# Performance work log

Hardware: AMD Instinct MI355X
Metric: run time of the kernel (lower is better)

Reference implementation:

```python
import jax, jax.numpy as jnp
import numpy as np


def ctc_neg_log_likelihood(log_probs, labels, input_lengths, label_lengths, blank=0):
    """Per-sample CTC negative log likelihood (torch.nn.CTCLoss semantics,
    zero_infinity=True). log_probs: (T, B, V) log-softmax; labels: (B, L) int."""
    T, B, V = log_probs.shape
    L = labels.shape[1]
    S = 2 * L + 1  # extended label sequence with interleaved blanks
    NEG = jnp.asarray(-1e9, log_probs.dtype)
    # extended labels: blank at even positions, label at odd positions -> (B, S)
    ext = jnp.full((B, S), blank, dtype=labels.dtype).at[:, 1::2].set(labels)
    # log prob of each extended symbol at each time: (T, B, S)
    lp_ext = jnp.take_along_axis(log_probs, jnp.broadcast_to(ext[None].astype(jnp.int32), (T, B, S)), axis=2)
    # skip transition s-2 -> s allowed iff ext[s] != blank and ext[s] != ext[s-2]
    skip = jnp.concatenate(
        [jnp.zeros((B, 2), bool), (ext[:, 2:] != blank) & (ext[:, 2:] != ext[:, :-2])], axis=1)
    alpha0 = jnp.full((B, S), NEG).at[:, 0].set(lp_ext[0, :, 0]).at[:, 1].set(lp_ext[0, :, 1])

    def step(alpha, inp):
        lp_t, t = inp
        s1 = jnp.concatenate([jnp.full((B, 1), NEG), alpha[:, :-1]], axis=1)
        s2 = jnp.where(skip, jnp.concatenate([jnp.full((B, 2), NEG), alpha[:, :-2]], axis=1), NEG)
        new = jnp.logaddexp(jnp.logaddexp(alpha, s1), s2) + lp_t
        # frames beyond each sample's input length leave alpha unchanged
        alpha = jnp.where((t < input_lengths)[:, None], new, alpha)
        return alpha, None

    alpha, _ = jax.lax.scan(step, alpha0, (lp_ext[1:], jnp.arange(1, T)))
    i1 = (2 * label_lengths.astype(jnp.int32) - 1)[:, None]
    a_last = jnp.take_along_axis(alpha, i1, axis=1)[:, 0]
    a_blank = jnp.take_along_axis(alpha, i1 + 1, axis=1)[:, 0]
    nll = -jnp.logaddexp(a_last, a_blank)
    # zero_infinity=True: infeasible alignments contribute 0
    return jnp.where(nll > 1e8, jnp.zeros_like(nll), nll)


def setup_inputs() -> dict:
    B, T, D, V, L = 32, 2048, 512, 5, 256
    key = jax.random.key(0)
    k1, k2, k3, k4, k5 = jax.random.split(key, 5)
    hs_pad = jax.random.normal(k1, (B, T, D), dtype=jnp.float32)
    W = jax.random.normal(k2, (D, V), dtype=jnp.float32) * 0.02
    b = jnp.zeros((V,), dtype=jnp.float32)
    hlens = jax.random.randint(k3, (B,), 1024, T + 1, dtype=jnp.int32)
    ys_pad = jax.random.randint(k4, (B, L), 1, V, dtype=jnp.int32)  # labels never equal blank=0
    ys_lens = jax.random.randint(k5, (B,), 64, L + 1, dtype=jnp.int32)
    return {"hs_pad": hs_pad, "W": W, "b": b, "hlens": hlens, "ys_pad": ys_pad, "ys_lens": ys_lens}


def reference(hs_pad, W, b, hlens, ys_pad, ys_lens):
    B = hs_pad.shape[0]
    logits = jnp.einsum('btd,dv->btv', hs_pad, W) + b      # ctc_lo (dropout p=0)
    logits_tbv = jnp.transpose(logits, (1, 0, 2))          # (T, B, V)
    log_probs = jax.nn.log_softmax(logits_tbv, axis=2)
    probs = jnp.exp(log_probs)                             # == softmax(logits)
    per_sample = ctc_neg_log_likelihood(log_probs, ys_pad, hlens, ys_lens, blank=0)
    loss = jnp.sum(per_sample) / B                         # sum-reduced CTC / batch size
    ys_hat = jnp.transpose(log_probs, (1, 0, 2))           # (B, T, V)
    no_log_ys_hat = jnp.transpose(probs, (1, 0, 2))        # (B, T, V)
    return loss, ys_hat, no_log_ys_hat
```

## Files before the change

### kernel.cpp

```cpp
#include <hip/hip_runtime.h>
#include <math.h>

#define B_DIM 32
#define T_DIM 2048
#define D_DIM 512
#define V_DIM 5
#define L_DIM 256
#define LN2D 0.6931471805599453
#define TP (T_DIM + 4)

typedef const float __attribute__((address_space(1)))* gas_fp;
typedef float __attribute__((address_space(3)))* las_fp;

__device__ __forceinline__ double dpp_shr1_f64(double x) {
    int lo = __double2loint(x), hi = __double2hiint(x);
    int slo = __builtin_amdgcn_update_dpp(0, lo, 0x138, 0xf, 0xf, true);
    int shi = __builtin_amdgcn_update_dpp(0, hi, 0x138, 0xf, 0xf, true);
    return __hiloint2double(shi, slo);
}
__device__ __forceinline__ int wave_imax_dpp(int e) {
    e = max(e, __builtin_amdgcn_update_dpp(0, e, 0x111, 0xf, 0xf, true));
    e = max(e, __builtin_amdgcn_update_dpp(0, e, 0x112, 0xf, 0xf, true));
    e = max(e, __builtin_amdgcn_update_dpp(0, e, 0x114, 0xf, 0xf, true));
    e = max(e, __builtin_amdgcn_update_dpp(0, e, 0x118, 0xf, 0xf, true));
    e = max(e, __builtin_amdgcn_update_dpp(0, e, 0x142, 0xf, 0xf, true));
    e = max(e, __builtin_amdgcn_update_dpp(0, e, 0x143, 0xf, 0xf, true));
    return __builtin_amdgcn_readlane(e, 63);
}
__device__ __forceinline__ float wave_fsum_dpp(float x) {
    x += __int_as_float(__builtin_amdgcn_update_dpp(0, __float_as_int(x), 0x111, 0xf, 0xf, true));
    x += __int_as_float(__builtin_amdgcn_update_dpp(0, __float_as_int(x), 0x112, 0xf, 0xf, true));
    x += __int_as_float(__builtin_amdgcn_update_dpp(0, __float_as_int(x), 0x114, 0xf, 0xf, true));
    x += __int_as_float(__builtin_amdgcn_update_dpp(0, __float_as_int(x), 0x118, 0xf, 0xf, true));
    x += __int_as_float(__builtin_amdgcn_update_dpp(0, __float_as_int(x), 0x142, 0xa, 0xf, false));
    x += __int_as_float(__builtin_amdgcn_update_dpp(0, __float_as_int(x), 0x143, 0xc, 0xf, false));
    return x;
}

__global__ __launch_bounds__(256) void k_logits_softmax(
    const float* __restrict__ hs, const float* __restrict__ W,
    const float* __restrict__ bias, float* __restrict__ logp,
    float* __restrict__ probs)
{
    const int lane = threadIdx.x & 63;
    const int wid  = (blockIdx.x * blockDim.x + threadIdx.x) >> 6;
    const int nwav = (gridDim.x * blockDim.x) >> 6;

    float wr[2][4][V_DIM];
#pragma unroll
    for (int c = 0; c < 2; ++c)
#pragma unroll
        for (int j = 0; j < 4; ++j) {
            const int k = c * 256 + lane * 4 + j;
#pragma unroll
            for (int v = 0; v < V_DIM; ++v) wr[c][j][v] = W[k * V_DIM + v];
        }
    float br[V_DIM];
#pragma unroll
    for (int v = 0; v < V_DIM; ++v) br[v] = bias[v];

    for (int row = wid; row < B_DIM * T_DIM; row += nwav) {
        const float* x = hs + (size_t)row * D_DIM;
        float4 xa = *reinterpret_cast<const float4*>(x + lane * 4);
        float4 xb = *reinterpret_cast<const float4*>(x + 256 + lane * 4);
        const float xs0[4] = {xa.x, xa.y, xa.z, xa.w};
        const float xs1[4] = {xb.x, xb.y, xb.z, xb.w};

        float acc[V_DIM];
#pragma unroll
        for (int v = 0; v < V_DIM; ++v) acc[v] = 0.f;
#pragma unroll
        for (int j = 0; j < 4; ++j)
#pragma unroll
            for (int v = 0; v < V_DIM; ++v) {
                acc[v] = fmaf(xs0[j], wr[0][j][v], acc[v]);
                acc[v] = fmaf(xs1[j], wr[1][j][v], acc[v]);
            }
#pragma unroll
        for (int v = 0; v < V_DIM; ++v) acc[v] = wave_fsum_dpp(acc[v]);

        if (lane == 63) {
#pragma unroll
            for (int v = 0; v < V_DIM; ++v) acc[v] += br[v];
            float m = fmaxf(fmaxf(fmaxf(acc[0], acc[1]), fmaxf(acc[2], acc[3])), acc[4]);
            float e[V_DIM], s = 0.f;
#pragma unroll
            for (int v = 0; v < V_DIM; ++v) { e[v] = __expf(acc[v] - m); s += e[v]; }
            float lse = m + __logf(s);
            float inv = 1.f / s;
            size_t base = (size_t)row * V_DIM;
#pragma unroll
            for (int v = 0; v < V_DIM; ++v) {
                logp[base + v]  = acc[v] - lse;
                probs[base + v] = e[v] * inv;
            }
        }
    }
}

__global__ __launch_bounds__(64) void k_ctc(
    const float* __restrict__ probs, const int* __restrict__ ys_pad,
    const int* __restrict__ hlens, const int* __restrict__ ys_lens,
    float* __restrict__ nll_out)
{
    __shared__ float  s_probs[T_DIM * V_DIM];
    __shared__ __align__(16) double s_pT[4][TP];
    __shared__ double s_alpha[513];
    __shared__ double s_red[64];

    const int b    = blockIdx.x;
    const int lane = threadIdx.x;
    const int hlen = hlens[b];
    const int lb   = ys_lens[b];
    const int Sb   = 2 * lb + 1;
    const float* pb = probs + (size_t)b * T_DIM * V_DIM;
    const int*  yrow = ys_pad + b * L_DIM;

    for (int i = 0; i < (T_DIM * V_DIM) / 64; ++i) {
        __builtin_amdgcn_global_load_lds((gas_fp)(pb + i * 64 + lane),
                                         (las_fp)(&s_probs[i * 64]), 4, 0, 0);
    }
    asm volatile("s_waitcnt vmcnt(0)" ::: "memory");

    double lg2 = 0.0;
    for (int i = 0; i < T_DIM / 64; ++i) {
        const int t = i * 64 + lane;
        const float* sp = &s_probs[t * 5];
        const float p0 = sp[0];
        const float inv = 1.0f / p0;
        s_pT[0][t + 3] = (double)(sp[1] * inv);
        s_pT[1][t + 3] = (double)(sp[2] * inv);
        s_pT[2][t + 3] = (double)(sp[3] * inv);
        s_pT[3][t + 3] = (double)(sp[4] * inv);
        if (t < hlen) {
            int ee; float mm = frexpf(p0, &ee);
            lg2 += (double)ee + (double)__log2f(mm);
        }
    }

    const int y0 = yrow[4 * lane + 0];
    const int y1 = yrow[4 * lane + 1];
    const int y2 = yrow[4 * lane + 2];
    const int y3 = yrow[4 * lane + 3];
    const int ym1 = (lane > 0) ? yrow[4 * lane - 1] : -1;

    const double sk0 = ((lane > 0) && (y0 != ym1)) ? 1.0 : 0.0;
    const double sk1 = (y1 != y0) ? 1.0 : 0.0;
    const double sk2 = (y2 != y1) ? 1.0 : 0.0;
    const double sk3 = (y3 != y2) ? 1.0 : 0.0;

    bool vmask[9];
#pragma unroll
    for (int i = 0; i < 9; ++i) vmask[i] = (8 * lane + i) < Sb;

    double aA[9], aB[9];
#pragma unroll
    for (int i = 0; i < 9; ++i) aA[i] = 0.0;
    if (lane == 0) {
        aA[0] = 1.0;
        aA[1] = s_pT[y0 - 1][3];
    }
    int E = 0;

    const double* q_y0 = &s_pT[y0 - 1][0];
    const double* q_y1 = &s_pT[y1 - 1][0];
    const double* q_y2 = &s_pT[y2 - 1][0];
    const double* q_y3 = &s_pT[y3 - 1][0];

#define LD4(d, p)                                                         \
    { double2 u0_ = *(const double2*)(p);                                 \
      double2 u1_ = *(const double2*)((p) + 2);                           \
      (d)[0] = u0_.x; (d)[1] = u0_.y; (d)[2] = u1_.x; (d)[3] = u1_.y; }

#define LOADQ(dst, kk)                                                    \
    { const int off_ = 4 + 4 * (kk);                                      \
      LD4(dst + 0,  q_y0 + off_); LD4(dst + 4,  q_y1 + off_);             \
      LD4(dst + 8,  q_y2 + off_); LD4(dst + 12, q_y3 + off_); }

#define STEPX(O, N, L, s_)                                                \
    {                                                                     \
        double p7_ = dpp_shr1_f64(O[7]);                                  \
        N[7] = fma(sk3, O[5], O[7] + O[6]) * L[12 + (s_)];                \
        N[2] = O[2] + O[1];                                               \
        N[3] = fma(sk1, O[1], O[3] + O[2]) * L[4 + (s_)];                 \
        N[4] = O[4] + O[3];                                               \
        N[5] = fma(sk2, O[3], O[5] + O[4]) * L[8 + (s_)];                 \
        N[6] = O[6] + O[5];                                               \
        N[8] = O[8] + O[7];                                               \
        N[0] = O[0] + p7_;                                                \
        N[1] = fma(sk0, p7_, O[1] + O[0]) * L[0 + (s_)];                  \
    }

#define STEP4(L)                                                          \
    STEPX(aA, aB, L, 0); STEPX(aB, aA, L, 1);                             \
    STEPX(aA, aB, L, 2); STEPX(aB, aA, L, 3);

#define RENORM()                                                          \
    {                                                                     \
        int hm_ = 0;                                                      \
        _Pragma("unroll")                                                 \
        for (int i_ = 0; i_ < 9; ++i_) {                                  \
            int h_ = __double2hiint(aA[i_]);                              \
            hm_ = vmask[i_] ? max(hm_, h_) : hm_;                         \
        }                                                                 \
        int em_ = wave_imax_dpp(hm_) >> 20;                               \
        if (em_ > 0) {                                                    \
            double sc_ = __hiloint2double((2046 - em_) << 20, 0);         \
            _Pragma("unroll")                                             \
            for (int i_ = 0; i_ < 9; ++i_) aA[i_] *= sc_;                 \
            E += em_ - 1023;                                              \
        }                                                                 \
    }

    const int NS = hlen - 1;
    const int nfull = NS >> 2;
    double lpA[16], lpB[16];
    LOADQ(lpA, 0);

    int blk = 0;
    for (; blk + 2 <= nfull; blk += 2) {
        LOADQ(lpB, blk + 1);
        STEP4(lpA);
        LOADQ(lpA, blk + 2);
        STEP4(lpB);
        if (blk & 2) RENORM();
    }
    if (blk < nfull) {
        STEP4(lpA);
    }
    for (int tt = 4 * nfull + 1; tt <= NS; ++tt) {
        double lt[16];
        lt[0]  = s_pT[y0 - 1][tt + 3];
        lt[4]  = s_pT[y1 - 1][tt + 3];
        lt[8]  = s_pT[y2 - 1][tt + 3];
        lt[12] = s_pT[y3 - 1][tt + 3];
        STEPX(aA, aB, lt, 0);
#pragma unroll
        for (int i = 0; i < 9; ++i) aA[i] = aB[i];
    }

#pragma unroll
    for (int i = 0; i < 8; ++i) s_alpha[8 * lane + i] = aA[i];
    if (lane == 63) s_alpha[512] = aA[8];
    s_red[lane] = lg2;
    __syncthreads();
    if (lane == 0) {
        double lg2tot = 0.0;
        for (int i = 0; i < 64; ++i) lg2tot += s_red[i];
        int i1 = 2 * lb - 1;
        double s = s_alpha[i1] + s_alpha[i1 + 1];
        double nlld = -(log(s) + ((double)E + lg2tot) * LN2D);
        float nll = (float)nlld;
        if (!(nll < 1e8f)) nll = 0.f;
        nll_out[b] = nll;
    }
#undef STEPX
#undef STEP4
#undef LOADQ
#undef LD4
#undef RENORM
}

__global__ __launch_bounds__(64) void k_finalize(
    const float* __restrict__ nll, float* __restrict__ out)
{
    int tid = threadIdx.x;
    float v = (tid < B_DIM) ? nll[tid] : 0.f;
#pragma unroll
    for (int off = 32; off; off >>= 1) v += __shfl_down(v, off, 64);
    if (tid == 0) out[0] = v / (float)B_DIM;
}

extern "C" void kernel_launch(void* const* d_in, const int* in_sizes, int n_in,
                              void* d_out, int out_size, void* d_ws, size_t ws_size,
                              hipStream_t stream) {
    const float* hs      = (const float*)d_in[0];
    const float* W       = (const float*)d_in[1];
    const float* bias    = (const float*)d_in[2];
    const int*   hlens   = (const int*)d_in[3];
    const int*   ys_pad  = (const int*)d_in[4];
    const int*   ys_lens = (const int*)d_in[5];

    float* out   = (float*)d_out;
    float* logp  = out + 1;
    float* probs = out + 1 + (size_t)B_DIM * T_DIM * V_DIM;
    float* nll   = (float*)d_ws;

    hipLaunchKernelGGL(k_logits_softmax, dim3(1024), dim3(256), 0, stream,
                       hs, W, bias, logp, probs);
    hipLaunchKernelGGL(k_ctc, dim3(B_DIM), dim3(64), 0, stream,
                       probs, ys_pad, hlens, ys_lens, nll);
    hipLaunchKernelGGL(k_finalize, dim3(1), dim3(64), 0, stream, nll, out);
}
```

Measured before the change: 143.6 us.

## Switch CTC forward recursion to fp32 with per-lane exponent scaling

Moves the CTC alpha recursion from double to float. Each lane now keeps its own power-of-two exponent, and the value shifted in from the neighbouring lane is corrected with ldexpf using the exponent difference between lanes. Renormalisation now runs every 8 steps as a lane-local operation instead of a wave-wide max reduction, and the final log-likelihood combines the two end states using their per-lane exponents. This targets the cost of fp64 arithmetic on the serial critical path and halves shared-memory traffic, but adds an ldexp per step and risks underflow or precision loss in float.

```diff
diff --git a/kernel.cpp b/kernel.cpp
--- a/kernel.cpp
+++ b/kernel.cpp
@@ -12,20 +12,12 @@
 typedef const float __attribute__((address_space(1)))* gas_fp;
 typedef float __attribute__((address_space(3)))* las_fp;
 
-__device__ __forceinline__ double dpp_shr1_f64(double x) {
-    int lo = __double2loint(x), hi = __double2hiint(x);
-    int slo = __builtin_amdgcn_update_dpp(0, lo, 0x138, 0xf, 0xf, true);
-    int shi = __builtin_amdgcn_update_dpp(0, hi, 0x138, 0xf, 0xf, true);
-    return __hiloint2double(shi, slo);
-}
-__device__ __forceinline__ int wave_imax_dpp(int e) {
-    e = max(e, __builtin_amdgcn_update_dpp(0, e, 0x111, 0xf, 0xf, true));
-    e = max(e, __builtin_amdgcn_update_dpp(0, e, 0x112, 0xf, 0xf, true));
-    e = max(e, __builtin_amdgcn_update_dpp(0, e, 0x114, 0xf, 0xf, true));
-    e = max(e, __builtin_amdgcn_update_dpp(0, e, 0x118, 0xf, 0xf, true));
-    e = max(e, __builtin_amdgcn_update_dpp(0, e, 0x142, 0xf, 0xf, true));
-    e = max(e, __builtin_amdgcn_update_dpp(0, e, 0x143, 0xf, 0xf, true));
-    return __builtin_amdgcn_readlane(e, 63);
+__device__ __forceinline__ float dpp_shr1_f32(float x) {
+    return __int_as_float(__builtin_amdgcn_update_dpp(
+        0, __float_as_int(x), 0x138, 0xf, 0xf, true));
+}
+__device__ __forceinline__ int dpp_shr1_i32(int x) {
+    return __builtin_amdgcn_update_dpp(0, x, 0x138, 0xf, 0xf, true);
 }
 __device__ __forceinline__ float wave_fsum_dpp(float x) {
     x += __int_as_float(__builtin_amdgcn_update_dpp(0, __float_as_int(x), 0x111, 0xf, 0xf, true));
@@ -104,8 +96,9 @@
     float* __restrict__ nll_out)
 {
     __shared__ float  s_probs[T_DIM * V_DIM];
-    __shared__ __align__(16) double s_pT[4][TP];
-    __shared__ double s_alpha[513];
+    __shared__ __align__(16) float s_pT[4][TP];
+    __shared__ float  s_beta[513];
+    __shared__ int    s_E[64];
     __shared__ double s_red[64];
 
     const int b    = blockIdx.x;
@@ -128,10 +121,10 @@
         const float* sp = &s_probs[t * 5];
         const float p0 = sp[0];
         const float inv = 1.0f / p0;
-        s_pT[0][t + 3] = (double)(sp[1] * inv);
-        s_pT[1][t + 3] = (double)(sp[2] * inv);
-        s_pT[2][t + 3] = (double)(sp[3] * inv);
-        s_pT[3][t + 3] = (double)(sp[4] * inv);
+        s_pT[0][t + 3] = sp[1] * inv;
+        s_pT[1][t + 3] = sp[2] * inv;
+        s_pT[2][t + 3] = sp[3] * inv;
+        s_pT[3][t + 3] = sp[4] * inv;
         if (t < hlen) {
             int ee; float mm = frexpf(p0, &ee);
             lg2 += (double)ee + (double)__log2f(mm);
@@ -144,51 +137,51 @@
     const int y3 = yrow[4 * lane + 3];
     const int ym1 = (lane > 0) ? yrow[4 * lane - 1] : -1;
 
-    const double sk0 = ((lane > 0) && (y0 != ym1)) ? 1.0 : 0.0;
-    const double sk1 = (y1 != y0) ? 1.0 : 0.0;
-    const double sk2 = (y2 != y1) ? 1.0 : 0.0;
-    const double sk3 = (y3 != y2) ? 1.0 : 0.0;
+    const float sk0 = ((lane > 0) && (y0 != ym1)) ? 1.f : 0.f;
+    const float sk1 = (y1 != y0) ? 1.f : 0.f;
+    const float sk2 = (y2 != y1) ? 1.f : 0.f;
+    const float sk3 = (y3 != y2) ? 1.f : 0.f;
 
     bool vmask[9];
 #pragma unroll
     for (int i = 0; i < 9; ++i) vmask[i] = (8 * lane + i) < Sb;
 
-    double aA[9], aB[9];
-#pragma unroll
-    for (int i = 0; i < 9; ++i) aA[i] = 0.0;
+    float aA[9], aB[9];
+#pragma unroll
+    for (int i = 0; i < 9; ++i) aA[i] = 0.f;
     if (lane == 0) {
-        aA[0] = 1.0;
+        aA[0] = 1.f;
         aA[1] = s_pT[y0 - 1][3];
     }
     int E = 0;
-
-    const double* q_y0 = &s_pT[y0 - 1][0];
-    const double* q_y1 = &s_pT[y1 - 1][0];
-    const double* q_y2 = &s_pT[y2 - 1][0];
-    const double* q_y3 = &s_pT[y3 - 1][0];
-
-#define LD4(d, p)                                                         \
-    { double2 u0_ = *(const double2*)(p);                                 \
-      double2 u1_ = *(const double2*)((p) + 2);                           \
-      (d)[0] = u0_.x; (d)[1] = u0_.y; (d)[2] = u1_.x; (d)[3] = u1_.y; }
+    int delta = 0;
+
+    const float* q_y0 = &s_pT[y0 - 1][0];
+    const float* q_y1 = &s_pT[y1 - 1][0];
+    const float* q_y2 = &s_pT[y2 - 1][0];
+    const float* q_y3 = &s_pT[y3 - 1][0];
+
+#define LD4F(d, p)                                                        \
+    { float4 u_ = *(const float4*)(p);                                    \
+      (d)[0] = u_.x; (d)[1] = u_.y; (d)[2] = u_.z; (d)[3] = u_.w; }
 
 #define LOADQ(dst, kk)                                                    \
     { const int off_ = 4 + 4 * (kk);                                      \
-      LD4(dst + 0,  q_y0 + off_); LD4(dst + 4,  q_y1 + off_);             \
-      LD4(dst + 8,  q_y2 + off_); LD4(dst + 12, q_y3 + off_); }
+      LD4F(dst + 0,  q_y0 + off_); LD4F(dst + 4,  q_y1 + off_);           \
+      LD4F(dst + 8,  q_y2 + off_); LD4F(dst + 12, q_y3 + off_); }
 
 #define STEPX(O, N, L, s_)                                                \
     {                                                                     \
-        double p7_ = dpp_shr1_f64(O[7]);                                  \
-        N[7] = fma(sk3, O[5], O[7] + O[6]) * L[12 + (s_)];                \
+        float p7_ = ldexpf(dpp_shr1_f32(O[7]), delta);                    \
+        N[7] = fmaf(sk3, O[5], O[7] + O[6]) * L[12 + (s_)];               \
         N[2] = O[2] + O[1];                                               \
-        N[3] = fma(sk1, O[1], O[3] + O[2]) * L[4 + (s_)];                 \
+        N[3] = fmaf(sk1, O[1], O[3] + O[2]) * L[4 + (s_)];                \
         N[4] = O[4] + O[3];                                               \
-        N[5] = fma(sk2, O[3], O[5] + O[4]) * L[8 + (s_)];                 \
+        N[5] = fmaf(sk2, O[3], O[5] + O[4]) * L[8 + (s_)];                \
         N[6] = O[6] + O[5];                                               \
         N[8] = O[8] + O[7];                                               \
         N[0] = O[0] + p7_;                                                \
-        N[1] = fma(sk0, p7_, O[1] + O[0]) * L[0 + (s_)];                  \
+        N[1] = fmaf(sk0, p7_, O[1] + O[0]) * L[0 + (s_)];                 \
     }
 
 #define STEP4(L)                                                          \
@@ -197,24 +190,30 @@
 
 #define RENORM()                                                          \
     {                                                                     \
-        int hm_ = 0;                                                      \
+        float m_ = 0.f;                                                   \
         _Pragma("unroll")                                                 \
-        for (int i_ = 0; i_ < 9; ++i_) {                                  \
-            int h_ = __double2hiint(aA[i_]);                              \
-            hm_ = vmask[i_] ? max(hm_, h_) : hm_;                         \
-        }                                                                 \
-        int em_ = wave_imax_dpp(hm_) >> 20;                               \
-        if (em_ > 0) {                                                    \
-            double sc_ = __hiloint2double((2046 - em_) << 20, 0);         \
-            _Pragma("unroll")                                             \
-            for (int i_ = 0; i_ < 9; ++i_) aA[i_] *= sc_;                 \
-            E += em_ - 1023;                                              \
-        }                                                                 \
+        for (int i_ = 0; i_ < 9; ++i_)                                    \
+            m_ = vmask[i_] ? fmaxf(m_, aA[i_]) : m_;                      \
+        const bool big_ = (m_ >= 1e-12f);                                 \
+        int em_ = (__float_as_int(m_) >> 23) & 0xff;                      \
+        em_ = em_ > 253 ? 253 : em_;                                      \
+        const float sc_ = __int_as_float((254 - (big_ ? em_ : 127)) << 23); \
+        _Pragma("unroll")                                                 \
+        for (int i_ = 0; i_ < 9; ++i_)                                    \
+            aA[i_] = big_ ? aA[i_] * sc_ : 0.f;                           \
+        const int En_ = E + (big_ ? em_ - 127 : 0);                       \
+        const int up_ = dpp_shr1_i32(En_);                                \
+        E = (!big_ && lane > 0) ? (up_ - 32) : En_;                       \
+        const int upE_ = dpp_shr1_i32(E);                                 \
+        int d_ = upE_ - E;                                                \
+        d_ = d_ > 52 ? 52 : d_;                                           \
+        d_ = d_ < -126 ? -126 : d_;                                       \
+        delta = d_;                                                       \
     }
 
     const int NS = hlen - 1;
     const int nfull = NS >> 2;
-    double lpA[16], lpB[16];
+    float lpA[16], lpB[16];
     LOADQ(lpA, 0);
 
     int blk = 0;
@@ -223,13 +222,13 @@
         STEP4(lpA);
         LOADQ(lpA, blk + 2);
         STEP4(lpB);
-        if (blk & 2) RENORM();
+        RENORM();
     }
     if (blk < nfull) {
         STEP4(lpA);
     }
     for (int tt = 4 * nfull + 1; tt <= NS; ++tt) {
-        double lt[16];
+        float lt[16];
         lt[0]  = s_pT[y0 - 1][tt + 3];
         lt[4]  = s_pT[y1 - 1][tt + 3];
         lt[8]  = s_pT[y2 - 1][tt + 3];
@@ -240,24 +239,30 @@
     }
 
 #pragma unroll
-    for (int i = 0; i < 8; ++i) s_alpha[8 * lane + i] = aA[i];
-    if (lane == 63) s_alpha[512] = aA[8];
+    for (int i = 0; i < 8; ++i) s_beta[8 * lane + i] = aA[i];
+    if (lane == 63) s_beta[512] = aA[8];
+    s_E[lane] = E;
     s_red[lane] = lg2;
     __syncthreads();
     if (lane == 0) {
         double lg2tot = 0.0;
         for (int i = 0; i < 64; ++i) lg2tot += s_red[i];
-        int i1 = 2 * lb - 1;
-        double s = s_alpha[i1] + s_alpha[i1 + 1];
-        double nlld = -(log(s) + ((double)E + lg2tot) * LN2D);
+        const int i1 = 2 * lb - 1, i2 = 2 * lb;
+        int l1 = i1 >> 3; if (l1 > 63) l1 = 63;
+        int l2 = i2 >> 3; if (l2 > 63) l2 = 63;
+        const int E1 = s_E[l1], E2 = s_E[l2];
+        const int Em = (E1 > E2) ? E1 : E2;
+        double s = ldexp((double)s_beta[i1], E1 - Em)
+                 + ldexp((double)s_beta[i2], E2 - Em);
+        double nlld = -(log(s) + ((double)Em + lg2tot) * LN2D);
         float nll = (float)nlld;
-        if (!(nll < 1e8f)) nll = 0.f;
+        if (!(fabsf(nll) < 1e8f)) nll = 0.f;
         nll_out[b] = nll;
     }
 #undef STEPX
 #undef STEP4
 #undef LOADQ
-#undef LD4
+#undef LD4F
 #undef RENORM
 }
 
```

New measurement: 143.6 us. No clear change (-0.0%).
